# Kernel optimization log

Hardware: AMD Instinct MI355X
Metric: run time of the kernel (lower is better)

The kernel has to match this reference:

```python
import jax, jax.numpy as jnp
import numpy as np

# Module hyperparameters (from init_kwargs)
L = 32        # spatial length
CIN = 128     # in_channels
COUT = 256    # out_channels
N = 8         # num_filters
STRIDE = 1
K = 9         # kernel_size (l//4+1 default for l>16)


def setup_inputs() -> dict:
    key = jax.random.key(0)
    kx, kw = jax.random.split(key)
    x = jax.random.normal(kx, (32, CIN, L, L), dtype=jnp.float32)
    # weight init: uniform in [-r, r], r = sqrt(1/(cin*k*k)), shape (n, cin//8, k, k)
    r = np.sqrt(1.0 / (CIN * K * K)).astype(np.float32)
    weight = (jax.random.uniform(kw, (N, CIN // 8, K, K), dtype=jnp.float32) - 0.5) * 2.0 * r
    return {"x": x, "weight": weight}


def reference(x, weight):
    # 3D real FFT over (channel, H, W) of the input: [B, CIN, L, L//2+1] complex
    x_hat = jnp.fft.rfftn(x, axes=(1, 2, 3))
    # Zero-pad weight (cin//8 -> CIN, k -> L) and transform: [N, CIN, L, L//2+1]
    w_hat = jnp.fft.rfftn(weight, s=(CIN, L, L))
    # Broadcast multiply (no channel reduction): [B, N, CIN, L, L//2+1]
    freq_out = jnp.einsum('bchw,nchw->bnchw', x_hat, w_hat)
    # Inverse 3D real FFT over (channel, H, W): [B, N, CIN, L, L]
    out = jnp.fft.irfftn(freq_out, axes=(2, 3, 4))
    # Channel shrink: keep every shrink_ratio-th channel -> CIN/shrink = COUT/N channels
    shrink_ratio = N * CIN // COUT
    out = out[:, :, ::shrink_ratio]                       # [B, N, COUT//N, L, L]
    out = out.reshape(out.shape[0], -1, out.shape[3], out.shape[4])  # [B, COUT, L, L]
    if STRIDE == 2:
        out = out[:, :, ::2, ::2]
    return out
```

## Files before the change

### kernel.cpp

```cpp
#include <hip/hip_runtime.h>

typedef __attribute__((ext_vector_type(4))) float  f32x4;
typedef __attribute__((ext_vector_type(8))) short  s16x8;

#define KK 9
#define NCHUNK 23

__device__ inline unsigned short f2bf(float f) {
    union { float f; unsigned int u; } v; v.f = f;
    unsigned int u = v.u + 0x7FFFu + ((v.u >> 16) & 1u);
    return (unsigned short)(u >> 16);
}

__global__ void prep_w(const float* __restrict__ wgt, unsigned short* __restrict__ Bg) {
    int idx = blockIdx.x * 256 + threadIdx.x;
    if (idx >= NCHUNK * 4 * 16 * 8) return;
    int e   = idx & 7;
    int col = (idx >> 3) & 15;
    int g   = (idx >> 7) & 3;
    int c   = idx >> 9;
    int pi   = g >> 1;
    int half = g & 1;
    int cp = half * 8 + e;
    int dc = 15 - cp;
    int q  = 2 * c + pi;
    int n  = col & 7;
    int t  = col >> 3;
    float val = 0.f;
    if (q <= 44) {
        int ky2 = q / 9;
        int kx  = q - 9 * ky2;
        int ky  = 2 * ky2 + t;
        if (ky <= 8)
            val = wgt[((n * 16 + dc) * KK + ky) * KK + kx];
    }
    Bg[idx] = f2bf(val);
}

__global__ __launch_bounds__(256) void fconv_mfma(
    const float* __restrict__ x,
    const unsigned short* __restrict__ Bg,
    float* __restrict__ out)
{
    __shared__ char smem[32768 + 4096];
    char*  smb     = smem;
    float* handoff = (float*)(smem + 32768);

    const int tid = threadIdx.x;
    const int b   = blockIdx.x >> 5;
    const int j   = blockIdx.x & 31;

    const float* xb = x + ((size_t)b << 17);
    int choff[16];
    #pragma unroll
    for (int i = 0; i < 16; ++i)
        choff[i] = ((4 * j - 15 + i) & 127) << 10;

    #pragma unroll
    for (int i = 0; i < 4; ++i) {
        int cell = i * 256 + tid;
        #pragma unroll
        for (int h = 0; h < 2; ++h) {
            union { unsigned short u16[8]; uint4 v; } pk;
            #pragma unroll
            for (int e = 0; e < 8; ++e)
                pk.u16[e] = f2bf(xb[choff[h * 8 + e] + cell]);
            *(uint4*)(smb + h * 16384 + cell * 16) = pk.v;
        }
    }
    __syncthreads();

    const int lane = tid & 63;
    const int wave = tid >> 6;
    const int r    = lane & 15;
    const int g    = lane >> 4;
    const int half = g & 1;
    const int pi   = g >> 1;
    const int y0   = wave * 8;

    f32x4 acc[8][2];
    #pragma unroll
    for (int dy = 0; dy < 8; ++dy) { acc[dy][0] = (f32x4)0.f; acc[dy][1] = (f32x4)0.f; }

    const char* bptr = (const char*)Bg + ((g * 16 + r) << 4);
    s16x8 bfrag = *(const s16x8*)(bptr);

    #pragma unroll 1
    for (int c = 0; c < NCHUNK; ++c) {
        int q   = 2 * c + pi;
        int ky2 = q / 9;
        int kx  = q - 9 * ky2;
        int wr  = (r - kx) & 31;
        int yb  = (y0 - 2 * ky2) & 31;
        int abase = (half << 14) + (wr << 4);

        int cn = (c < NCHUNK - 1) ? c + 1 : NCHUNK - 1;
        s16x8 bnext = *(const s16x8*)(bptr + (cn << 10));

        #pragma unroll
        for (int dy = 0; dy < 8; ++dy) {
            int yy = (yb + dy) & 31;
            int ra = abase + (yy << 9);
            s16x8 a0 = *(const s16x8*)(smb + ra);
            s16x8 a1 = *(const s16x8*)(smb + (ra ^ 256));
            acc[dy][0] = __builtin_amdgcn_mfma_f32_16x16x32_bf16(a0, bfrag, acc[dy][0], 0, 0, 0);
            acc[dy][1] = __builtin_amdgcn_mfma_f32_16x16x32_bf16(a1, bfrag, acc[dy][1], 0, 0, 0);
        }
        bfrag = bnext;
    }

    float recv[8][2][4];
    #pragma unroll
    for (int dy = 0; dy < 8; ++dy)
        #pragma unroll
        for (int h = 0; h < 2; ++h)
            #pragma unroll
            for (int i = 0; i < 4; ++i)
                recv[dy][h][i] = __shfl_xor(acc[dy][h][i], 8);

    if (r < 8) {
        #pragma unroll
        for (int h = 0; h < 2; ++h)
            *(f32x4*)&handoff[wave * 256 + r * 32 + h * 16 + g * 4] = *(f32x4*)recv[7][h];
    }
    __syncthreads();

    if (r < 8) {
        const int pw = (wave + 3) & 3;
        f32x4 prev[2];
        #pragma unroll
        for (int h = 0; h < 2; ++h)
            prev[h] = *(f32x4*)&handoff[pw * 256 + r * 32 + h * 16 + g * 4];

        float* ob = out + (((size_t)(b * 256 + r * 32 + j)) << 10) + (g << 2);
        #pragma unroll
        for (int dy = 0; dy < 8; ++dy) {
            #pragma unroll
            for (int h = 0; h < 2; ++h) {
                f32x4 t1 = (dy == 0) ? prev[h] : *(f32x4*)recv[dy - 1][h];
                f32x4 v  = acc[dy][h] + t1;
                *(f32x4*)(ob + (y0 + dy) * 32 + h * 16) = v;
            }
        }
    }
}

__global__ __launch_bounds__(256, 2) void fconv_fallback(
    const float* __restrict__ x,
    const float* __restrict__ wgt,
    float* __restrict__ out)
{
    __shared__ float sw[16 * KK * KK * 8];
    const int tid = threadIdx.x;
    for (int idx = tid; idx < 8 * 16 * KK * KK; idx += 256) {
        int n  = idx / (16 * KK * KK);
        int rm = idx - n * (16 * KK * KK);
        int dc = rm / (KK * KK);
        int r2 = rm - dc * (KK * KK);
        int ky = r2 / KK;
        int kx = r2 - ky * KK;
        sw[((dc * KK + kx) * KK + ky) * 8 + n] = wgt[idx];
    }
    __syncthreads();

    const int bid = blockIdx.x;
    const int b   = bid >> 6;
    const int j   = (bid >> 1) & 31;
    const int yh  = bid & 1;
    const int xw  = tid & 31;
    const int yg  = tid >> 5;
    const int y_base = yh * 16 + yg * 2;

    int rows[10];
    #pragma unroll
    for (int i = 0; i < 10; ++i)
        rows[i] = ((y_base + 24 + i) & 31) << 5;

    float acc[8][2];
    #pragma unroll
    for (int n = 0; n < 8; ++n) { acc[n][0] = 0.f; acc[n][1] = 0.f; }

    const int c0 = 4 * j;
    #pragma unroll 1
    for (int dc = 0; dc < 16; ++dc) {
        const int c_src = (c0 - dc) & 127;
        const float* bx = x + (((size_t)b * 128 + c_src) << 10);
        #pragma unroll 1
        for (int kx = 0; kx < KK; ++kx) {
            const int x_col = (xw - kx) & 31;
            float win[10];
            #pragma unroll
            for (int i = 0; i < 10; ++i)
                win[i] = bx[rows[i] + x_col];
            const float4* wp = (const float4*)&sw[((dc * KK + kx) * KK) * 8];
            #pragma unroll
            for (int ky = 0; ky < KK; ++ky) {
                float4 wA = wp[2 * ky];
                float4 wB = wp[2 * ky + 1];
                float x0 = win[8 - ky];
                float x1 = win[9 - ky];
                acc[0][0] += x0 * wA.x; acc[0][1] += x1 * wA.x;
                acc[1][0] += x0 * wA.y; acc[1][1] += x1 * wA.y;
                acc[2][0] += x0 * wA.z; acc[2][1] += x1 * wA.z;
                acc[3][0] += x0 * wA.w; acc[3][1] += x1 * wA.w;
                acc[4][0] += x0 * wB.x; acc[4][1] += x1 * wB.x;
                acc[5][0] += x0 * wB.y; acc[5][1] += x1 * wB.y;
                acc[6][0] += x0 * wB.z; acc[6][1] += x1 * wB.z;
                acc[7][0] += x0 * wB.w; acc[7][1] += x1 * wB.w;
            }
        }
    }
    #pragma unroll
    for (int n = 0; n < 8; ++n) {
        float* op = out + ((((size_t)b * 256) + n * 32 + j) << 10) + (y_base << 5) + xw;
        op[0]  = acc[n][0];
        op[32] = acc[n][1];
    }
}

extern "C" void kernel_launch(void* const* d_in, const int* in_sizes, int n_in,
                              void* d_out, int out_size, void* d_ws, size_t ws_size,
                              hipStream_t stream) {
    const float* x   = (const float*)d_in[0];
    const float* w   = (const float*)d_in[1];
    float*       out = (float*)d_out;

    const size_t BG_BYTES = NCHUNK * 4 * 16 * 8 * sizeof(unsigned short);
    if (ws_size >= BG_BYTES) {
        unsigned short* Bg = (unsigned short*)d_ws;
        prep_w<<<46, 256, 0, stream>>>(w, Bg);
        fconv_mfma<<<1024, 256, 0, stream>>>(x, Bg, out);
    } else {
        fconv_fallback<<<2048, 256, 0, stream>>>(x, w, out);
    }
}
```

Baseline: 113.3 us.

## Add 32x32x16 MFMA conv path with 512-thread blocks and direct output

Adds a new main path that uses 32x32x16 bf16 MFMA instead of 16x16x32. The weights are repacked into 108 chunks that put four output-row offsets into the N dimension, so each wave computes four output rows directly. This removes the cross-lane shuffle and shared-memory handoff of partial rows, and blocks grow to 512 threads with 8 waves. The trade-offs are more wasted zero-padded weight work, since the ky range is padded to 12 per kx, and a larger workspace requirement.

```diff
diff --git a/kernel.cpp b/kernel.cpp
--- a/kernel.cpp
+++ b/kernel.cpp
@@ -1,7 +1,8 @@
 #include <hip/hip_runtime.h>
 
-typedef __attribute__((ext_vector_type(4))) float  f32x4;
-typedef __attribute__((ext_vector_type(8))) short  s16x8;
+typedef __attribute__((ext_vector_type(4)))  float f32x4;
+typedef __attribute__((ext_vector_type(16))) float f32x16;
+typedef __attribute__((ext_vector_type(8)))  short s16x8;
 
 #define KK 9
 #define NCHUNK 23
@@ -10,6 +11,92 @@
     union { float f; unsigned int u; } v; v.f = f;
     unsigned int u = v.u + 0x7FFFu + ((v.u >> 16) & 1u);
     return (unsigned short)(u >> 16);
+}
+
+
+__global__ void prep_w32(const float* __restrict__ wgt, unsigned short* __restrict__ Bg) {
+    int idx = blockIdx.x * 256 + threadIdx.x;
+    if (idx >= 108 * 64 * 8) return;
+    int e     = idx & 7;
+    int lanei = (idx >> 3) & 63;
+    int chunk = idx >> 9;
+    int col   = lanei & 31;
+    int khalf = lanei >> 5;
+    int n  = col & 7;
+    int p  = col >> 3;
+    int kx = chunk / 12;
+    int s  = chunk - 12 * kx;
+    int ky = s - 3 + p;
+    int cp = khalf * 8 + e;
+    int dc = 15 - cp;
+    float val = 0.f;
+    if (ky >= 0 && ky <= 8)
+        val = wgt[((n * 16 + dc) * KK + ky) * KK + kx];
+    Bg[idx] = f2bf(val);
+}
+
+__global__ __launch_bounds__(512, 8) void fconv_mfma32(
+    const float* __restrict__ x,
+    const unsigned short* __restrict__ Bg,
+    float* __restrict__ out)
+{
+    __shared__ char smb[32768];
+
+    const int tid = threadIdx.x;
+    const int b   = blockIdx.x >> 5;
+    const int j   = blockIdx.x & 31;
+
+    const float* xb = x + ((size_t)b << 17);
+    int choff[16];
+    #pragma unroll
+    for (int i = 0; i < 16; ++i)
+        choff[i] = ((4 * j - 15 + i) & 127) << 10;
+
+    #pragma unroll
+    for (int i = 0; i < 2; ++i) {
+        int cell = i * 512 + tid;
+        #pragma unroll
+        for (int h = 0; h < 2; ++h) {
+            union { unsigned short u16[8]; uint4 v; } pk;
+            #pragma unroll
+            for (int e = 0; e < 8; ++e)
+                pk.u16[e] = f2bf(xb[choff[h * 8 + e] + cell]);
+            *(uint4*)(smb + h * 16384 + cell * 16) = pk.v;
+        }
+    }
+    __syncthreads();
+
+    const int lane  = tid & 63;
+    const int wave  = tid >> 6;
+    const int wrow  = lane & 31;
+    const int khalf = lane >> 5;
+    const int g4    = wave * 4;
+
+    f32x16 acc = (f32x16)0.f;
+    const char* bp = (const char*)Bg + (lane << 4);
+
+    #pragma unroll 1
+    for (int kx = 0; kx < 9; ++kx) {
+        const int abase = (khalf << 14) + (((wrow - kx) & 31) << 4);
+        const char* bpk = bp + ((kx * 12) << 10);
+        #pragma unroll
+        for (int s = 0; s < 12; ++s) {
+            int yp = (g4 + 3 - s) & 31;
+            s16x8 a  = *(const s16x8*)(smb + abase + (yp << 9));
+            s16x8 bb = *(const s16x8*)(bpk + (s << 10));
+            acc = __builtin_amdgcn_mfma_f32_32x32x16_bf16(a, bb, acc, 0, 0, 0);
+        }
+    }
+
+    const int n = wrow & 7;
+    const int p = wrow >> 3;
+    float* ob = out + (((size_t)(b * 256 + n * 32 + j)) << 10)
+                    + ((g4 + p) << 5) + 4 * khalf;
+    #pragma unroll
+    for (int q = 0; q < 4; ++q) {
+        f32x4 v = { acc[4*q], acc[4*q+1], acc[4*q+2], acc[4*q+3] };
+        *(f32x4*)(ob + q * 8) = v;
+    }
 }
 
 __global__ void prep_w(const float* __restrict__ wgt, unsigned short* __restrict__ Bg) {
@@ -225,8 +312,14 @@
     const float* w   = (const float*)d_in[1];
     float*       out = (float*)d_out;
 
-    const size_t BG_BYTES = NCHUNK * 4 * 16 * 8 * sizeof(unsigned short);
-    if (ws_size >= BG_BYTES) {
+    const size_t BG32_BYTES = (size_t)108 * 64 * 8 * sizeof(unsigned short);
+    const size_t BG16_BYTES = (size_t)NCHUNK * 4 * 16 * 8 * sizeof(unsigned short);
+
+    if (ws_size >= BG32_BYTES) {
+        unsigned short* Bg = (unsigned short*)d_ws;
+        prep_w32<<<216, 256, 0, stream>>>(w, Bg);
+        fconv_mfma32<<<1024, 512, 0, stream>>>(x, Bg, out);
+    } else if (ws_size >= BG16_BYTES) {
         unsigned short* Bg = (unsigned short*)d_ws;
         prep_w<<<46, 256, 0, stream>>>(w, Bg);
         fconv_mfma<<<1024, 256, 0, stream>>>(x, Bg, out);
```

New measurement: 113.0 us. Within noise of the previous version (-0.2%).
